# Kernel optimization log

Hardware: AMD Instinct MI355X
Metric: run time of the kernel (lower is better)

The kernel has to match this reference:

```python
import jax, jax.numpy as jnp
import numpy as np

RADIUS, HEAD, SLOT, DIM = 16.0, 8, 112, 512

def _l2norm(x, axis):
    n = jnp.linalg.norm(x, axis=axis, keepdims=True)
    return x / jnp.maximum(n, 1e-12)

def _layernorm(x, g, b, eps=1e-5):
    mu = jnp.mean(x, axis=-1, keepdims=True)
    var = jnp.mean((x - mu) ** 2, axis=-1, keepdims=True)
    return (x - mu) / jnp.sqrt(var + eps) * g + b

def setup_inputs() -> dict:
    key = jax.random.key(0)
    ks = jax.random.split(key, 12)
    B, S = 32, 512
    return {
        "query": jax.random.normal(ks[0], (B, S, DIM), jnp.float32),
        "value": jax.random.normal(ks[1], (B, S, DIM), jnp.float32),
        "key_mem": jax.random.normal(ks[2], (HEAD * SLOT, DIM // HEAD), jnp.float32) * 0.5,
        "value_mem": jax.random.normal(ks[3], (SLOT, DIM), jnp.float32) * 0.5,
        "Wq": jax.random.normal(ks[4], (DIM, DIM), jnp.float32) * 0.02,
        "bq": jnp.zeros((DIM,), jnp.float32),
        "Wv": jax.random.normal(ks[5], (DIM, DIM), jnp.float32) * 0.02,
        "bv": jnp.zeros((DIM,), jnp.float32),
        "Wl": jax.random.normal(ks[6], (DIM, DIM * HEAD), jnp.float32) * 0.02,
        "bl": jnp.zeros((DIM,), jnp.float32),
        "g1": jnp.ones((DIM,), jnp.float32), "b1": jnp.zeros((DIM,), jnp.float32),
        "g2": jnp.ones((DIM,), jnp.float32), "b2": jnp.zeros((DIM,), jnp.float32),
        "g3": jnp.ones((DIM,), jnp.float32), "b3": jnp.zeros((DIM,), jnp.float32),
    }

def reference(query, value, key_mem, value_mem, Wq, bq, Wv, bv, Wl, bl,
              g1, b1, g2, b2, g3, b3):
    B, S, C = query.shape
    mq = query.reshape(B * S, C)                                   # (BS, 512)
    # --- key addressing (read path) ---
    key_norm = _l2norm(key_mem.reshape(HEAD, SLOT, -1), axis=2)    # (h, s, 64)
    eq = _l2norm((mq @ Wq.T + bq).reshape(B * S, HEAD, -1), axis=2)
    key_sim = jnp.einsum('bhd,hsd->bhs', eq, key_norm)             # (BS, h, s)
    key_add = jax.nn.softmax(RADIUS * key_sim, axis=2)
    m_head = jnp.einsum('bhs,sd->bhd', key_add,
                        jax.lax.stop_gradient(value_mem))          # (BS, h, 512)
    vir = _layernorm(m_head.reshape(B * S, HEAD * DIM) @ Wl.T + bl, g2, b2)
    te_fusion = _layernorm(query + vir.reshape(B, S, DIM), g1, b1)  # dropout = eval identity
    # --- value addressing (write/train path) ---
    mv = value.reshape(B * S, DIM)
    ev = jax.lax.stop_gradient(mv) @ Wv.T + bv
    value_norm = _l2norm(value_mem, axis=1)                        # (s, 512)
    value_sim = _l2norm(ev, axis=1) @ value_norm.T                 # (BS, s)
    value_add = jax.nn.softmax(RADIUS * value_sim, axis=1)
    aud = value_add @ value_mem                                    # (BS, 512)
    contrastive = 0.5 * jnp.abs(jnp.eye(SLOT, dtype=value_norm.dtype)
                                - value_norm @ value_norm.T).sum()[None]
    mvd = jax.lax.stop_gradient(mv)
    cos = (aud * mvd).sum(1) / jnp.maximum(
        jnp.linalg.norm(aud, axis=1) * jnp.linalg.norm(mvd, axis=1), 1e-8)
    recon = jnp.abs(1.0 - cos).reshape(B, S).sum(1)                # (B,)
    aud = _layernorm(aud, g3, b3)
    tr_fusion = _layernorm(query + aud.reshape(B, S, DIM), g1, b1)
    return (te_fusion, tr_fusion, recon, contrastive)
```

## Files before the change

### kernel.cpp

```cpp
#include <hip/hip_runtime.h>
#include <math.h>

#define DIMC   512
#define HEADS  8
#define SLOTS  112
#define HD     64
#define NROWS  16384
#define RADIUSF 16.0f

typedef short short8 __attribute__((ext_vector_type(8)));
typedef unsigned short ushort8 __attribute__((ext_vector_type(8)));
typedef float f32x4  __attribute__((ext_vector_type(4)));

__device__ __forceinline__ unsigned short f2bf(float f)
{
    unsigned u = __float_as_uint(f);
    unsigned r = (u + 0x7FFFu + ((u >> 16) & 1u)) >> 16;
    return (unsigned short)r;
}
__device__ __forceinline__ float bf2f(unsigned short h)
{
    return __uint_as_float((unsigned)h << 16);
}

__device__ __forceinline__ void gl16(const void* g, void* lds_wave_base)
{
    __builtin_amdgcn_global_load_lds(
        (const __attribute__((address_space(1))) unsigned int*)g,
        (__attribute__((address_space(3))) unsigned int*)lds_wave_base,
        16, 0, 0);
}

#define DPP_ADD(x, ctrl, rmask)                                               \
    (x) += __int_as_float(__builtin_amdgcn_update_dpp(                        \
               0, __float_as_int(x), (ctrl), (rmask), 0xf, true))

__device__ __forceinline__ float wsum64(float x)
{
    DPP_ADD(x, 0x111, 0xf);
    DPP_ADD(x, 0x112, 0xf);
    DPP_ADD(x, 0x114, 0xf);
    DPP_ADD(x, 0x118, 0xf);
    DPP_ADD(x, 0x142, 0xa);
    DPP_ADD(x, 0x143, 0xc);
    return __int_as_float(__builtin_amdgcn_readlane(__float_as_int(x), 63));
}

__device__ __forceinline__ void wsum64_4(float& a, float& b, float& c, float& d)
{
    DPP_ADD(a, 0x111, 0xf); DPP_ADD(b, 0x111, 0xf); DPP_ADD(c, 0x111, 0xf); DPP_ADD(d, 0x111, 0xf);
    DPP_ADD(a, 0x112, 0xf); DPP_ADD(b, 0x112, 0xf); DPP_ADD(c, 0x112, 0xf); DPP_ADD(d, 0x112, 0xf);
    DPP_ADD(a, 0x114, 0xf); DPP_ADD(b, 0x114, 0xf); DPP_ADD(c, 0x114, 0xf); DPP_ADD(d, 0x114, 0xf);
    DPP_ADD(a, 0x118, 0xf); DPP_ADD(b, 0x118, 0xf); DPP_ADD(c, 0x118, 0xf); DPP_ADD(d, 0x118, 0xf);
    DPP_ADD(a, 0x142, 0xa); DPP_ADD(b, 0x142, 0xa); DPP_ADD(c, 0x142, 0xa); DPP_ADD(d, 0x142, 0xa);
    DPP_ADD(a, 0x143, 0xc); DPP_ADD(b, 0x143, 0xc); DPP_ADD(c, 0x143, 0xc); DPP_ADD(d, 0x143, 0xc);
    a = __int_as_float(__builtin_amdgcn_readlane(__float_as_int(a), 63));
    b = __int_as_float(__builtin_amdgcn_readlane(__float_as_int(b), 63));
    c = __int_as_float(__builtin_amdgcn_readlane(__float_as_int(c), 63));
    d = __int_as_float(__builtin_amdgcn_readlane(__float_as_int(d), 63));
}

__global__ __launch_bounds__(256)
void gemm_bf16(const short* __restrict__ A, int lda,
               const short* __restrict__ B, int ldb,
               float* __restrict__ C, unsigned short* __restrict__ Cb,
               int ldc, int K, const float* __restrict__ bias, int Nvalid,
               int aZ, int bZ, int cZ)
{
    __shared__ short As[128 * 32];
    __shared__ short Bs[128 * 32];
    A += (size_t)blockIdx.z * aZ;
    B += (size_t)blockIdx.z * bZ;
    const size_t czoff = (size_t)blockIdx.z * cZ;
    const int tid  = threadIdx.x;
    const int wave = tid >> 6;
    const int lane = tid & 63;
    const int m0 = blockIdx.y * 128;
    const int n0 = blockIdx.x * 128;
    const int wm = (wave >> 1) * 64;
    const int wn = (wave & 1) * 64;

    const int srow = tid >> 2;
    const int schk = (tid & 3) * 8;

    const int fr = lane & 15;
    const int fq = (lane >> 4) * 8;

    f32x4 acc[4][4] = {};

    const short* Ag = A + (size_t)(m0 + srow) * lda + schk;
    const short* Bg = B + (size_t)(n0 + srow) * ldb + schk;

    short* asL = As + wave * 512;
    short* asU = As + 2048 + wave * 512;
    short* bsL = Bs + wave * 512;
    short* bsU = Bs + 2048 + wave * 512;

    for (int k0 = 0; k0 < K; k0 += 32) {
        gl16(Ag, asL);
        gl16(Ag + (size_t)64 * lda, asU);
        gl16(Bg, bsL);
        gl16(Bg + (size_t)64 * ldb, bsU);
        Ag += 32; Bg += 32;
        __syncthreads();
        short8 af[4], bf[4];
        #pragma unroll
        for (int i = 0; i < 4; ++i)
            af[i] = *(const short8*)&As[(wm + i * 16 + fr) * 32 + fq];
        #pragma unroll
        for (int j = 0; j < 4; ++j)
            bf[j] = *(const short8*)&Bs[(wn + j * 16 + fr) * 32 + fq];
        #pragma unroll
        for (int i = 0; i < 4; ++i)
            #pragma unroll
            for (int j = 0; j < 4; ++j)
                acc[i][j] = __builtin_amdgcn_mfma_f32_16x16x32_bf16(
                    af[i], bf[j], acc[i][j], 0, 0, 0);
        __syncthreads();
    }

    const int cr = (lane >> 4) * 4;
    const int cc = lane & 15;
    #pragma unroll
    for (int i = 0; i < 4; ++i) {
        const int grow = m0 + wm + i * 16 + cr;
        #pragma unroll
        for (int j = 0; j < 4; ++j) {
            const int gcol = n0 + wn + j * 16 + cc;
            if (gcol < Nvalid) {
                const float bb = bias ? bias[gcol] : 0.f;
                const size_t base = czoff + (size_t)grow * ldc + gcol;
                #pragma unroll
                for (int r = 0; r < 4; ++r) {
                    const float val = acc[i][j][r] + bb;
                    if (C)  C[base + (size_t)r * ldc]  = val;
                    if (Cb) Cb[base + (size_t)r * ldc] = f2bf(val);
                }
            }
        }
    }
}

__global__ __launch_bounds__(256)
void gemm_softmax(const short* __restrict__ A, int lda, int aZ,
                  const short* __restrict__ B, int ldb, int bZ,
                  int K,
                  unsigned short* __restrict__ Ob, int ldo, int oPerZ, int padN)
{
    __shared__ short As[128 * 32];
    __shared__ short Bs[128 * 32];
    __shared__ float P[128][113];
    __shared__ float hinvS[128];
    A += (size_t)blockIdx.z * aZ;
    B += (size_t)blockIdx.z * bZ;
    const int tid  = threadIdx.x;
    const int wave = tid >> 6;
    const int lane = tid & 63;
    const int m0 = blockIdx.y * 128;
    const int wm = (wave >> 1) * 64;
    const int wn = (wave & 1) * 64;
    const int srow = tid >> 2;
    const int schk = (tid & 3) * 8;
    const int fr = lane & 15;
    const int fq = (lane >> 4) * 8;

    f32x4 acc[4][4] = {};
    float ss[4] = {0.f, 0.f, 0.f, 0.f};

    const short* Ag = A + (size_t)(m0 + srow) * lda + schk;
    const short* Bg = B + (size_t)srow * ldb + schk;

    short* asL = As + wave * 512;
    short* asU = As + 2048 + wave * 512;
    short* bsL = Bs + wave * 512;
    short* bsU = Bs + 2048 + wave * 512;

    for (int k0 = 0; k0 < K; k0 += 32) {
        gl16(Ag, asL);
        gl16(Ag + (size_t)64 * lda, asU);
        gl16(Bg, bsL);
        gl16(Bg + (size_t)64 * ldb, bsU);
        Ag += 32; Bg += 32;
        __syncthreads();
        short8 af[4], bf[4];
        #pragma unroll
        for (int i = 0; i < 4; ++i)
            af[i] = *(const short8*)&As[(wm + i * 16 + fr) * 32 + fq];
        #pragma unroll
        for (int j = 0; j < 4; ++j)
            bf[j] = *(const short8*)&Bs[(wn + j * 16 + fr) * 32 + fq];
        #pragma unroll
        for (int i = 0; i < 4; ++i)
            #pragma unroll
            for (int e = 0; e < 8; ++e) {
                const float f = bf2f((unsigned short)af[i][e]);
                ss[i] += f * f;
            }
        #pragma unroll
        for (int i = 0; i < 4; ++i)
            #pragma unroll
            for (int j = 0; j < 4; ++j)
                acc[i][j] = __builtin_amdgcn_mfma_f32_16x16x32_bf16(
                    af[i], bf[j], acc[i][j], 0, 0, 0);
        __syncthreads();
    }

    #pragma unroll
    for (int i = 0; i < 4; ++i) {
        ss[i] += __shfl_xor(ss[i], 16, 64);
        ss[i] += __shfl_xor(ss[i], 32, 64);
    }
    if (lane < 16) {
        #pragma unroll
        for (int i = 0; i < 4; ++i)
            hinvS[wm + i * 16 + lane] = 1.f / fmaxf(sqrtf(ss[i]), 1e-12f);
    }

    const int cr = (lane >> 4) * 4;
    const int cc = lane & 15;
    #pragma unroll
    for (int i = 0; i < 4; ++i) {
        const int prow = wm + i * 16 + cr;
        #pragma unroll
        for (int j = 0; j < 4; ++j) {
            const int pcol = wn + j * 16 + cc;
            if (pcol < SLOTS) {
                #pragma unroll
                for (int r = 0; r < 4; ++r)
                    P[prow + r][pcol] = acc[i][j][r];
            }
        }
    }
    __syncthreads();

    const int rowt = tid >> 1;
    const int half = tid & 1;
    const int k0 = half * 56;
    const int rr = m0 + rowt;
    const float s = RADIUSF * hinvS[rowt];
    float mx = -1e30f;
    for (int k = k0; k < k0 + 56; ++k) mx = fmaxf(mx, P[rowt][k]);
    mx = fmaxf(mx, __shfl_xor(mx, 1, 64));
    float sum = 0.f;
    for (int k = k0; k < k0 + 56; ++k) {
        const float e = __expf(s * (P[rowt][k] - mx));
        P[rowt][k] = e;
        sum += e;
    }
    sum += __shfl_xor(sum, 1, 64);
    const float inv = 1.f / sum;
    unsigned short* orow = Ob + (size_t)rr * ldo + (size_t)blockIdx.z * oPerZ;
    for (int k = k0; k < k0 + 56; ++k) orow[k] = f2bf(P[rowt][k] * inv);
    if (half == 1)
        for (int k = SLOTS; k < padN; ++k) orow[k] = 0;
}

__device__ __forceinline__ float block_sum_256(float v, float* red)
{
    #pragma unroll
    for (int off = 32; off; off >>= 1) v += __shfl_down(v, off, 64);
    const int lane = threadIdx.x & 63, wid = threadIdx.x >> 6;
    __syncthreads();
    if (lane == 0) red[wid] = v;
    __syncthreads();
    return red[0] + red[1] + red[2] + red[3];
}

__global__ void conv_all(const float* __restrict__ q, const float* __restrict__ v,
                         const float* __restrict__ Wq, const float* __restrict__ Wv,
                         const float* __restrict__ Wl, const float* __restrict__ vm,
                         unsigned short* __restrict__ qbf, unsigned short* __restrict__ vbf,
                         unsigned short* __restrict__ wqbf, unsigned short* __restrict__ wvbf,
                         unsigned short* __restrict__ wlbf, unsigned short* __restrict__ vmbf)
{
    const int i = blockIdx.x * blockDim.x + threadIdx.x;
    const float* src;
    unsigned short* dst;
    int off;
    if (i < 2097152)      { src = q;  dst = qbf;  off = i; }
    else if (i < 4194304) { src = v;  dst = vbf;  off = i - 2097152; }
    else if (i < 4259840) { src = Wq; dst = wqbf; off = i - 4194304; }
    else if (i < 4325376) { src = Wv; dst = wvbf; off = i - 4259840; }
    else if (i < 4849664) { src = Wl; dst = wlbf; off = i - 4325376; }
    else if (i < 4864000) { src = vm; dst = vmbf; off = i - 4849664; }
    else {
        const int j = i - 4864000;
        *(ushort4*)(vmbf + 57344 + (size_t)j * 4) = make_ushort4(0, 0, 0, 0);
        return;
    }
    const float4 x = *(const float4*)(src + (size_t)off * 4);
    ushort4 o;
    o.x = f2bf(x.x); o.y = f2bf(x.y); o.z = f2bf(x.z); o.w = f2bf(x.w);
    *(ushort4*)(dst + (size_t)off * 4) = o;
}

__global__ void prep_key_norm(const float* __restrict__ km,
                              unsigned short* __restrict__ knb,
                              float* __restrict__ outrc)
{
    const int row = blockIdx.x;
    const int h = row >> 7, s = row & 127;
    const int lane = threadIdx.x;
    if (row == 0 && lane < 33) outrc[lane] = 0.f;
    const float v = (s < SLOTS) ? km[(size_t)(h * SLOTS + s) * HD + lane] : 0.f;
    const float ssum = wsum64(v * v);
    const float inv = 1.f / fmaxf(sqrtf(ssum), 1e-12f);
    knb[(size_t)row * HD + lane] = f2bf(v * inv);
}

__global__ void prep_value_norm(const float* __restrict__ vm,
                                float* __restrict__ vn,
                                unsigned short* __restrict__ vnb,
                                unsigned short* __restrict__ vmTb)
{
    const int row = blockIdx.x;
    const int tid = threadIdx.x;
    if (row >= 112) {
        const int idx = (row - 112) * 256 + tid;
        if (idx < 8192) {
            vmTb[(size_t)(idx >> 4) * 128 + 112 + (idx & 15)] = 0;
        } else {
            const int j = idx - 8192;
            vnb[(size_t)(112 + (j >> 9)) * 512 + (j & 511)] = 0;
        }
        return;
    }
    __shared__ float red[4];
    const float v0 = vm[(size_t)row * DIMC + tid];
    const float v1 = vm[(size_t)row * DIMC + 256 + tid];
    const float tot = block_sum_256(v0 * v0 + v1 * v1, red);
    const float inv = 1.f / fmaxf(sqrtf(tot), 1e-12f);
    vn[(size_t)row * DIMC + tid]        = v0 * inv;
    vn[(size_t)row * DIMC + 256 + tid]  = v1 * inv;
    vnb[(size_t)row * DIMC + tid]       = f2bf(v0 * inv);
    vnb[(size_t)row * DIMC + 256 + tid] = f2bf(v1 * inv);
    vmTb[(size_t)tid * 128 + row]         = f2bf(v0);
    vmTb[(size_t)(256 + tid) * 128 + row] = f2bf(v1);
}

__global__ void contrastive_kernel(const float* __restrict__ vn, float* __restrict__ outc)
{
    __shared__ float vni[DIMC];
    __shared__ float red[2];
    const int i = blockIdx.x, tid = threadIdx.x;
    for (int d = tid; d < DIMC; d += 128) vni[d] = vn[(size_t)i * DIMC + d];
    __syncthreads();
    float t = 0.f;
    if (tid < SLOTS) {
        const float* r = vn + (size_t)tid * DIMC;
        float dot = 0.f;
        for (int d = 0; d < DIMC; ++d) dot += vni[d] * r[d];
        const float delta = (tid == i) ? 1.f : 0.f;
        t = fabsf(delta - dot);
    }
    #pragma unroll
    for (int off = 32; off; off >>= 1) t += __shfl_down(t, off, 64);
    if ((tid & 63) == 0) red[tid >> 6] = t;
    __syncthreads();
    if (tid == 0) atomicAdd(outc, 0.5f * (red[0] + red[1]));
}

__global__ __launch_bounds__(256, 4)
void vir_te_w(const float* __restrict__ vir_pre, const float* __restrict__ query,
              const float* __restrict__ g1, const float* __restrict__ b1,
              const float* __restrict__ g2, const float* __restrict__ b2,
              float* __restrict__ out_te)
{
    const int wave = threadIdx.x >> 6, lane = threadIdx.x & 63;
    const int r0 = blockIdx.x * 8 + wave * 2;
    const int c0 = lane * 8;

    float x[2][8], q[2][8];
    #pragma unroll
    for (int p = 0; p < 2; ++p) {
        const size_t base = (size_t)(r0 + p) * DIMC + c0;
        *(f32x4*)&x[p][0] = *(const f32x4*)(vir_pre + base);
        *(f32x4*)&x[p][4] = *(const f32x4*)(vir_pre + base + 4);
        *(f32x4*)&q[p][0] = *(const f32x4*)(query + base);
        *(f32x4*)&q[p][4] = *(const f32x4*)(query + base + 4);
    }
    float gg2[8], bb2[8], gg1[8], bb1[8];
    *(f32x4*)&gg2[0] = *(const f32x4*)(g2 + c0);
    *(f32x4*)&gg2[4] = *(const f32x4*)(g2 + c0 + 4);
    *(f32x4*)&bb2[0] = *(const f32x4*)(b2 + c0);
    *(f32x4*)&bb2[4] = *(const f32x4*)(b2 + c0 + 4);
    *(f32x4*)&gg1[0] = *(const f32x4*)(g1 + c0);
    *(f32x4*)&gg1[4] = *(const f32x4*)(g1 + c0 + 4);
    *(f32x4*)&bb1[0] = *(const f32x4*)(b1 + c0);
    *(f32x4*)&bb1[4] = *(const f32x4*)(b1 + c0 + 4);

    float s1[2] = {0.f, 0.f}, s2[2] = {0.f, 0.f};
    #pragma unroll
    for (int p = 0; p < 2; ++p)
        #pragma unroll
        for (int i = 0; i < 8; ++i) {
            s1[p] += x[p][i];
            s2[p] += x[p][i] * x[p][i];
        }
    wsum64_4(s1[0], s2[0], s1[1], s2[1]);

    float y[2][8];
    float t1[2] = {0.f, 0.f}, t2[2] = {0.f, 0.f};
    #pragma unroll
    for (int p = 0; p < 2; ++p) {
        const float mu = s1[p] * (1.f / DIMC);
        const float var = s2[p] * (1.f / DIMC) - mu * mu;
        const float rstd = rsqrtf(var + 1e-5f);
        #pragma unroll
        for (int i = 0; i < 8; ++i) {
            const float v = (x[p][i] - mu) * rstd * gg2[i] + bb2[i];
            y[p][i] = q[p][i] + v;
            t1[p] += y[p][i];
            t2[p] += y[p][i] * y[p][i];
        }
    }
    wsum64_4(t1[0], t2[0], t1[1], t2[1]);

    #pragma unroll
    for (int p = 0; p < 2; ++p) {
        const float mu = t1[p] * (1.f / DIMC);
        const float var = t2[p] * (1.f / DIMC) - mu * mu;
        const float rstd = rsqrtf(var + 1e-5f);
        float o[8];
        #pragma unroll
        for (int i = 0; i < 8; ++i)
            o[i] = (y[p][i] - mu) * rstd * gg1[i] + bb1[i];
        const size_t base = (size_t)(r0 + p) * DIMC + c0;
        *(float4*)(out_te + base)     = make_float4(o[0], o[1], o[2], o[3]);
        *(float4*)(out_te + base + 4) = make_float4(o[4], o[5], o[6], o[7]);
    }
}

__global__ __launch_bounds__(256, 4)
void aud_epilogue_w(const float* __restrict__ aud, const float* __restrict__ value,
                    const float* __restrict__ query,
                    const float* __restrict__ g1, const float* __restrict__ b1,
                    const float* __restrict__ g3, const float* __restrict__ b3,
                    float* __restrict__ out_tr, float* __restrict__ recon)
{
    __shared__ float red[4];
    const int wave = threadIdx.x >> 6, lane = threadIdx.x & 63;
    const int r0 = blockIdx.x * 8 + wave * 2;
    const int c0 = lane * 8;

    float a[2][8], v[2][8], q[2][8];
    #pragma unroll
    for (int p = 0; p < 2; ++p) {
        const size_t base = (size_t)(r0 + p) * DIMC + c0;
        *(f32x4*)&a[p][0] = *(const f32x4*)(aud + base);
        *(f32x4*)&a[p][4] = *(const f32x4*)(aud + base + 4);
        *(f32x4*)&v[p][0] = *(const f32x4*)(value + base);
        *(f32x4*)&v[p][4] = *(const f32x4*)(value + base + 4);
        *(f32x4*)&q[p][0] = *(const f32x4*)(query + base);
        *(f32x4*)&q[p][4] = *(const f32x4*)(query + base + 4);
    }
    float gg3[8], bb3[8], gg1[8], bb1[8];
    *(f32x4*)&gg3[0] = *(const f32x4*)(g3 + c0);
    *(f32x4*)&gg3[4] = *(const f32x4*)(g3 + c0 + 4);
    *(f32x4*)&bb3[0] = *(const f32x4*)(b3 + c0);
    *(f32x4*)&bb3[4] = *(const f32x4*)(b3 + c0 + 4);
    *(f32x4*)&gg1[0] = *(const f32x4*)(g1 + c0);
    *(f32x4*)&gg1[4] = *(const f32x4*)(g1 + c0 + 4);
    *(f32x4*)&bb1[0] = *(const f32x4*)(b1 + c0);
    *(f32x4*)&bb1[4] = *(const f32x4*)(b1 + c0 + 4);

    float dot[2] = {0.f, 0.f}, na[2] = {0.f, 0.f};
    float nv[2] = {0.f, 0.f}, s1[2] = {0.f, 0.f};
    #pragma unroll
    for (int p = 0; p < 2; ++p)
        #pragma unroll
        for (int i = 0; i < 8; ++i) {
            dot[p] += a[p][i] * v[p][i];
            na[p]  += a[p][i] * a[p][i];
            nv[p]  += v[p][i] * v[p][i];
            s1[p]  += a[p][i];
        }
    wsum64_4(dot[0], na[0], nv[0], s1[0]);
    wsum64_4(dot[1], na[1], nv[1], s1[1]);

    float rloc = 0.f;
    #pragma unroll
    for (int p = 0; p < 2; ++p) {
        const float cosv = dot[p] / fmaxf(sqrtf(na[p]) * sqrtf(nv[p]), 1e-8f);
        rloc += fabsf(1.f - cosv);
    }
    if (lane == 0) red[wave] = rloc;

    float y[2][8];
    float t1[2] = {0.f, 0.f}, t2[2] = {0.f, 0.f};
    #pragma unroll
    for (int p = 0; p < 2; ++p) {
        const float mu = s1[p] * (1.f / DIMC);
        const float var = na[p] * (1.f / DIMC) - mu * mu;
        const float rstd = rsqrtf(var + 1e-5f);
        #pragma unroll
        for (int i = 0; i < 8; ++i) {
            const float w = (a[p][i] - mu) * rstd * gg3[i] + bb3[i];
            y[p][i] = q[p][i] + w;
            t1[p] += y[p][i];
            t2[p] += y[p][i] * y[p][i];
        }
    }
    wsum64_4(t1[0], t2[0], t1[1], t2[1]);

    #pragma unroll
    for (int p = 0; p < 2; ++p) {
        const float mu = t1[p] * (1.f / DIMC);
        const float var = t2[p] * (1.f / DIMC) - mu * mu;
        const float rstd = rsqrtf(var + 1e-5f);
        float o[8];
        #pragma unroll
        for (int i = 0; i < 8; ++i)
            o[i] = (y[p][i] - mu) * rstd * gg1[i] + bb1[i];
        const size_t base = (size_t)(r0 + p) * DIMC + c0;
        *(float4*)(out_tr + base)     = make_float4(o[0], o[1], o[2], o[3]);
        *(float4*)(out_tr + base + 4) = make_float4(o[4], o[5], o[6], o[7]);
    }

    __syncthreads();
    if (threadIdx.x == 0)
        atomicAdd(&recon[r0 >> 9], red[0] + red[1] + red[2] + red[3]);
}

extern "C" void kernel_launch(void* const* d_in, const int* in_sizes, int n_in,
                              void* d_out, int out_size, void* d_ws, size_t ws_size,
                              hipStream_t stream)
{
    const float* query = (const float*)d_in[0];
    const float* value = (const float*)d_in[1];
    const float* keym  = (const float*)d_in[2];
    const float* vmem  = (const float*)d_in[3];
    const float* Wq    = (const float*)d_in[4];
    const float* bq    = (const float*)d_in[5];
    const float* Wv    = (const float*)d_in[6];
    const float* bv    = (const float*)d_in[7];
    const float* Wl    = (const float*)d_in[8];
    const float* bl    = (const float*)d_in[9];
    const float* g1    = (const float*)d_in[10];
    const float* b1    = (const float*)d_in[11];
    const float* g2    = (const float*)d_in[12];
    const float* b2    = (const float*)d_in[13];
    const float* g3    = (const float*)d_in[14];
    const float* b3    = (const float*)d_in[15];

    float* out    = (float*)d_out;
    float* out_te = out;
    float* out_tr = out + 8388608;
    float* out_rc = out + 16777216;

    float* ws = (float*)d_ws;
    unsigned short* w_knb  = (unsigned short*)(ws + 0);
    unsigned short* w_vmTb = (unsigned short*)(ws + 32768);
    unsigned short* w_vnb  = (unsigned short*)(ws + 65536);
    float*          w_vn   = ws + 98304;
    unsigned short* w_w2tbf= (unsigned short*)(ws + 155648);
    unsigned short* w_vmbf = (unsigned short*)(ws + 516096);
    unsigned short* w_wlbf = (unsigned short*)(ws + 548864);
    float*          w_big1 = ws + 1597440;
    unsigned short* w_xbf  = (unsigned short*)(ws + 9986048);
    unsigned short* w_kaddc= (unsigned short*)(ws + 14180352);
    unsigned short* w_vsb  = (unsigned short*)(ws + 21520384);
    unsigned short* w_qbf  = (unsigned short*)(ws + 22568960);
    unsigned short* w_vbf  = (unsigned short*)(ws + 26763264);
    unsigned short* w_wqbf = (unsigned short*)(ws + 30957568);
    unsigned short* w_wvbf = (unsigned short*)(ws + 31088640);

    conv_all<<<19008, 256, 0, stream>>>(query, value, Wq, Wv, Wl, vmem,
                                        w_qbf, w_vbf, w_wqbf, w_wvbf,
                                        w_wlbf, w_vmbf);
    prep_key_norm<<<1024, 64, 0, stream>>>(keym, w_knb, out_rc);
    prep_value_norm<<<176, 256, 0, stream>>>(vmem, w_vn, w_vnb, w_vmTb);
    contrastive_kernel<<<112, 128, 0, stream>>>(w_vn, out_rc + 32);
    gemm_bf16<<<dim3(1, 4, 8), 256, 0, stream>>>(
        (const short*)w_wlbf, HEADS * DIMC, (const short*)w_vmbf, DIMC,
        nullptr, w_w2tbf, HEADS * SLOTS, DIMC, nullptr, SLOTS,
        DIMC, 0, SLOTS);

    gemm_bf16<<<dim3(4, 128), 256, 0, stream>>>(
        (const short*)w_qbf, DIMC, (const short*)w_wqbf, DIMC,
        nullptr, w_xbf, DIMC, DIMC, bq, DIMC, 0, 0, 0);
    gemm_softmax<<<dim3(1, 128, 8), 256, 0, stream>>>(
        (const short*)w_xbf, DIMC, HD, (const short*)w_knb, HD, 128 * HD,
        HD, w_kaddc, HEADS * SLOTS, SLOTS, SLOTS);
    gemm_bf16<<<dim3(4, 128), 256, 0, stream>>>(
        (const short*)w_kaddc, HEADS * SLOTS, (const short*)w_w2tbf, HEADS * SLOTS,
        w_big1, nullptr, DIMC, HEADS * SLOTS, bl, DIMC, 0, 0, 0);
    vir_te_w<<<NROWS / 8, 256, 0, stream>>>(w_big1, query, g1, b1, g2, b2, out_te);

    gemm_bf16<<<dim3(4, 128), 256, 0, stream>>>(
        (const short*)w_vbf, DIMC, (const short*)w_wvbf, DIMC,
        nullptr, w_xbf, DIMC, DIMC, bv, DIMC, 0, 0, 0);
    gemm_softmax<<<dim3(1, 128, 1), 256, 0, stream>>>(
        (const short*)w_xbf, DIMC, 0, (const short*)w_vnb, DIMC, 0,
        DIMC, w_vsb, 128, 0, 128);
    gemm_bf16<<<dim3(4, 128), 256, 0, stream>>>(
        (const short*)w_vsb, 128, (const short*)w_vmTb, 128,
        w_big1, nullptr, DIMC, 128, nullptr, DIMC, 0, 0, 0);
    aud_epilogue_w<<<NROWS / 8, 256, 0, stream>>>(
        w_big1, value, query, g1, b1, g3, b3, out_tr, out_rc);
}
```

Measured before the change: 359.8 us.

## Fuse output GEMMs with layernorm epilogues into full-row-tile kernels

```diff
diff --git a/kernel.cpp b/kernel.cpp
--- a/kernel.cpp
+++ b/kernel.cpp
@@ -255,6 +255,246 @@
         for (int k = SLOTS; k < padN; ++k) orow[k] = 0;
 }
 
+
+#define FUSED_GEMM_CORE(A, lda, B, ldb, K)                                    \
+    f32x4 acc[2][8] = {};                                                     \
+    {                                                                         \
+        const int lrow = lane >> 2;                                           \
+        const int lchk = (lane & 3) * 8;                                      \
+        const short* Ag = (A) + (size_t)(m0 + wave * 16 + lrow) * (lda) + lchk;\
+        const short* Bg = (B) + (size_t)(wave * 16 + lrow) * (ldb) + lchk;    \
+        short* asB = As + wave * 512;                                         \
+        short* bsB = Bs + wave * 512;                                         \
+        for (int k0 = 0; k0 < (K); k0 += 32) {                                \
+            if (wave < 2) gl16(Ag, asB);                                      \
+            _Pragma("unroll")                                                 \
+            for (int s = 0; s < 8; ++s)                                       \
+                gl16(Bg + (size_t)(s * 64) * (ldb), bsB + s * 2048);          \
+            Ag += 32; Bg += 32;                                               \
+            __syncthreads();                                                  \
+            short8 af[2], bf[8];                                              \
+            af[0] = *(const short8*)&As[fr * 32 + fq];                        \
+            af[1] = *(const short8*)&As[(16 + fr) * 32 + fq];                 \
+            _Pragma("unroll")                                                 \
+            for (int c = 0; c < 8; ++c)                                       \
+                bf[c] = *(const short8*)&Bs[(wave * 128 + c * 16 + fr) * 32 + fq];\
+            _Pragma("unroll")                                                 \
+            for (int i = 0; i < 2; ++i)                                       \
+                _Pragma("unroll")                                             \
+                for (int c = 0; c < 8; ++c)                                   \
+                    acc[i][c] = __builtin_amdgcn_mfma_f32_16x16x32_bf16(      \
+                        af[i], bf[c], acc[i][c], 0, 0, 0);                    \
+            __syncthreads();                                                  \
+        }                                                                     \
+    }                                                                         \
+    {                                                                         \
+        const int cr = (lane >> 4) * 4;                                       \
+        const int cc = lane & 15;                                             \
+        _Pragma("unroll")                                                     \
+        for (int i = 0; i < 2; ++i)                                           \
+            _Pragma("unroll")                                                 \
+            for (int c = 0; c < 8; ++c) {                                     \
+                const int col = wave * 128 + c * 16 + cc;                     \
+                _Pragma("unroll")                                             \
+                for (int r = 0; r < 4; ++r)                                   \
+                    P[(i * 16 + cr + r) * 516 + col] = acc[i][c][r];          \
+            }                                                                 \
+    }                                                                         \
+    __syncthreads();
+
+__global__ __launch_bounds__(256)
+void gemm_vir_te(const short* __restrict__ A, int lda,
+                 const short* __restrict__ B, int ldb, int K,
+                 const float* __restrict__ bias, const float* __restrict__ query,
+                 const float* __restrict__ g1, const float* __restrict__ b1,
+                 const float* __restrict__ g2, const float* __restrict__ b2,
+                 float* __restrict__ out_te)
+{
+    __shared__ float P[32 * 516];
+    short* As = (short*)P;
+    short* Bs = As + 1024;
+    const int tid = threadIdx.x;
+    const int wave = tid >> 6;
+    const int lane = tid & 63;
+    const int m0 = blockIdx.x * 32;
+    const int fr = lane & 15;
+    const int fq = (lane >> 4) * 8;
+
+    FUSED_GEMM_CORE(A, lda, B, ldb, K)
+
+    const int c0 = lane * 8;
+    float blv[8], gg2[8], bb2[8], gg1[8], bb1[8];
+    *(f32x4*)&blv[0] = *(const f32x4*)(bias + c0);
+    *(f32x4*)&blv[4] = *(const f32x4*)(bias + c0 + 4);
+    *(f32x4*)&gg2[0] = *(const f32x4*)(g2 + c0);
+    *(f32x4*)&gg2[4] = *(const f32x4*)(g2 + c0 + 4);
+    *(f32x4*)&bb2[0] = *(const f32x4*)(b2 + c0);
+    *(f32x4*)&bb2[4] = *(const f32x4*)(b2 + c0 + 4);
+    *(f32x4*)&gg1[0] = *(const f32x4*)(g1 + c0);
+    *(f32x4*)&gg1[4] = *(const f32x4*)(g1 + c0 + 4);
+    *(f32x4*)&bb1[0] = *(const f32x4*)(b1 + c0);
+    *(f32x4*)&bb1[4] = *(const f32x4*)(b1 + c0 + 4);
+
+    for (int rp = 0; rp < 4; ++rp) {
+        const int lr0 = rp * 8 + wave * 2;
+        float x[2][8], q[2][8];
+        #pragma unroll
+        for (int p = 0; p < 2; ++p) {
+            *(f32x4*)&x[p][0] = *(const f32x4*)&P[(lr0 + p) * 516 + c0];
+            *(f32x4*)&x[p][4] = *(const f32x4*)&P[(lr0 + p) * 516 + c0 + 4];
+            const size_t gbase = (size_t)(m0 + lr0 + p) * DIMC + c0;
+            *(f32x4*)&q[p][0] = *(const f32x4*)(query + gbase);
+            *(f32x4*)&q[p][4] = *(const f32x4*)(query + gbase + 4);
+            #pragma unroll
+            for (int j = 0; j < 8; ++j) x[p][j] += blv[j];
+        }
+        float s1[2] = {0.f, 0.f}, s2[2] = {0.f, 0.f};
+        #pragma unroll
+        for (int p = 0; p < 2; ++p)
+            #pragma unroll
+            for (int j = 0; j < 8; ++j) {
+                s1[p] += x[p][j];
+                s2[p] += x[p][j] * x[p][j];
+            }
+        wsum64_4(s1[0], s2[0], s1[1], s2[1]);
+
+        float y[2][8];
+        float t1[2] = {0.f, 0.f}, t2[2] = {0.f, 0.f};
+        #pragma unroll
+        for (int p = 0; p < 2; ++p) {
+            const float mu = s1[p] * (1.f / DIMC);
+            const float var = s2[p] * (1.f / DIMC) - mu * mu;
+            const float rstd = rsqrtf(var + 1e-5f);
+            #pragma unroll
+            for (int j = 0; j < 8; ++j) {
+                const float v = (x[p][j] - mu) * rstd * gg2[j] + bb2[j];
+                y[p][j] = q[p][j] + v;
+                t1[p] += y[p][j];
+                t2[p] += y[p][j] * y[p][j];
+            }
+        }
+        wsum64_4(t1[0], t2[0], t1[1], t2[1]);
+
+        #pragma unroll
+        for (int p = 0; p < 2; ++p) {
+            const float mu = t1[p] * (1.f / DIMC);
+            const float var = t2[p] * (1.f / DIMC) - mu * mu;
+            const float rstd = rsqrtf(var + 1e-5f);
+            float o[8];
+            #pragma unroll
+            for (int j = 0; j < 8; ++j)
+                o[j] = (y[p][j] - mu) * rstd * gg1[j] + bb1[j];
+            const size_t gbase = (size_t)(m0 + lr0 + p) * DIMC + c0;
+            *(float4*)(out_te + gbase)     = make_float4(o[0], o[1], o[2], o[3]);
+            *(float4*)(out_te + gbase + 4) = make_float4(o[4], o[5], o[6], o[7]);
+        }
+    }
+}
+
+__global__ __launch_bounds__(256)
+void gemm_aud_tr(const short* __restrict__ A, int lda,
+                 const short* __restrict__ B, int ldb, int K,
+                 const float* __restrict__ value, const float* __restrict__ query,
+                 const float* __restrict__ g1, const float* __restrict__ b1,
+                 const float* __restrict__ g3, const float* __restrict__ b3,
+                 float* __restrict__ out_tr, float* __restrict__ recon)
+{
+    __shared__ float P[32 * 516];
+    __shared__ float red[4];
+    short* As = (short*)P;
+    short* Bs = As + 1024;
+    const int tid = threadIdx.x;
+    const int wave = tid >> 6;
+    const int lane = tid & 63;
+    const int m0 = blockIdx.x * 32;
+    const int fr = lane & 15;
+    const int fq = (lane >> 4) * 8;
+
+    FUSED_GEMM_CORE(A, lda, B, ldb, K)
+
+    const int c0 = lane * 8;
+    float gg3[8], bb3[8], gg1[8], bb1[8];
+    *(f32x4*)&gg3[0] = *(const f32x4*)(g3 + c0);
+    *(f32x4*)&gg3[4] = *(const f32x4*)(g3 + c0 + 4);
+    *(f32x4*)&bb3[0] = *(const f32x4*)(b3 + c0);
+    *(f32x4*)&bb3[4] = *(const f32x4*)(b3 + c0 + 4);
+    *(f32x4*)&gg1[0] = *(const f32x4*)(g1 + c0);
+    *(f32x4*)&gg1[4] = *(const f32x4*)(g1 + c0 + 4);
+    *(f32x4*)&bb1[0] = *(const f32x4*)(b1 + c0);
+    *(f32x4*)&bb1[4] = *(const f32x4*)(b1 + c0 + 4);
+
+    float rloc = 0.f;
+    for (int rp = 0; rp < 4; ++rp) {
+        const int lr0 = rp * 8 + wave * 2;
+        float a[2][8], v[2][8], q[2][8];
+        #pragma unroll
+        for (int p = 0; p < 2; ++p) {
+            *(f32x4*)&a[p][0] = *(const f32x4*)&P[(lr0 + p) * 516 + c0];
+            *(f32x4*)&a[p][4] = *(const f32x4*)&P[(lr0 + p) * 516 + c0 + 4];
+            const size_t gbase = (size_t)(m0 + lr0 + p) * DIMC + c0;
+            *(f32x4*)&v[p][0] = *(const f32x4*)(value + gbase);
+            *(f32x4*)&v[p][4] = *(const f32x4*)(value + gbase + 4);
+            *(f32x4*)&q[p][0] = *(const f32x4*)(query + gbase);
+            *(f32x4*)&q[p][4] = *(const f32x4*)(query + gbase + 4);
+        }
+        float dot[2] = {0.f, 0.f}, na[2] = {0.f, 0.f};
+        float nv[2] = {0.f, 0.f}, s1[2] = {0.f, 0.f};
+        #pragma unroll
+        for (int p = 0; p < 2; ++p)
+            #pragma unroll
+            for (int j = 0; j < 8; ++j) {
+                dot[p] += a[p][j] * v[p][j];
+                na[p]  += a[p][j] * a[p][j];
+                nv[p]  += v[p][j] * v[p][j];
+                s1[p]  += a[p][j];
+            }
+        wsum64_4(dot[0], na[0], nv[0], s1[0]);
+        wsum64_4(dot[1], na[1], nv[1], s1[1]);
+
+        #pragma unroll
+        for (int p = 0; p < 2; ++p) {
+            const float cosv = dot[p] / fmaxf(sqrtf(na[p]) * sqrtf(nv[p]), 1e-8f);
+            rloc += fabsf(1.f - cosv);
+        }
+
+        float y[2][8];
+        float t1[2] = {0.f, 0.f}, t2[2] = {0.f, 0.f};
+        #pragma unroll
+        for (int p = 0; p < 2; ++p) {
+            const float mu = s1[p] * (1.f / DIMC);
+            const float var = na[p] * (1.f / DIMC) - mu * mu;
+            const float rstd = rsqrtf(var + 1e-5f);
+            #pragma unroll
+            for (int j = 0; j < 8; ++j) {
+                const float w = (a[p][j] - mu) * rstd * gg3[j] + bb3[j];
+                y[p][j] = q[p][j] + w;
+                t1[p] += y[p][j];
+                t2[p] += y[p][j] * y[p][j];
+            }
+        }
+        wsum64_4(t1[0], t2[0], t1[1], t2[1]);
+
+        #pragma unroll
+        for (int p = 0; p < 2; ++p) {
+            const float mu = t1[p] * (1.f / DIMC);
+            const float var = t2[p] * (1.f / DIMC) - mu * mu;
+            const float rstd = rsqrtf(var + 1e-5f);
+            float o[8];
+            #pragma unroll
+            for (int j = 0; j < 8; ++j)
+                o[j] = (y[p][j] - mu) * rstd * gg1[j] + bb1[j];
+            const size_t gbase = (size_t)(m0 + lr0 + p) * DIMC + c0;
+            *(float4*)(out_tr + gbase)     = make_float4(o[0], o[1], o[2], o[3]);
+            *(float4*)(out_tr + gbase + 4) = make_float4(o[4], o[5], o[6], o[7]);
+        }
+    }
+
+    if (lane == 0) red[wave] = rloc;
+    __syncthreads();
+    if (tid == 0)
+        atomicAdd(&recon[m0 >> 9], red[0] + red[1] + red[2] + red[3]);
+}
+
 __device__ __forceinline__ float block_sum_256(float v, float* red)
 {
     #pragma unroll
@@ -358,168 +598,6 @@
     if ((tid & 63) == 0) red[tid >> 6] = t;
     __syncthreads();
     if (tid == 0) atomicAdd(outc, 0.5f * (red[0] + red[1]));
-}
-
-__global__ __launch_bounds__(256, 4)
-void vir_te_w(const float* __restrict__ vir_pre, const float* __restrict__ query,
-              const float* __restrict__ g1, const float* __restrict__ b1,
-              const float* __restrict__ g2, const float* __restrict__ b2,
-              float* __restrict__ out_te)
-{
-    const int wave = threadIdx.x >> 6, lane = threadIdx.x & 63;
-    const int r0 = blockIdx.x * 8 + wave * 2;
-    const int c0 = lane * 8;
-
-    float x[2][8], q[2][8];
-    #pragma unroll
-    for (int p = 0; p < 2; ++p) {
-        const size_t base = (size_t)(r0 + p) * DIMC + c0;
-        *(f32x4*)&x[p][0] = *(const f32x4*)(vir_pre + base);
-        *(f32x4*)&x[p][4] = *(const f32x4*)(vir_pre + base + 4);
-        *(f32x4*)&q[p][0] = *(const f32x4*)(query + base);
-        *(f32x4*)&q[p][4] = *(const f32x4*)(query + base + 4);
-    }
-    float gg2[8], bb2[8], gg1[8], bb1[8];
-    *(f32x4*)&gg2[0] = *(const f32x4*)(g2 + c0);
-    *(f32x4*)&gg2[4] = *(const f32x4*)(g2 + c0 + 4);
-    *(f32x4*)&bb2[0] = *(const f32x4*)(b2 + c0);
-    *(f32x4*)&bb2[4] = *(const f32x4*)(b2 + c0 + 4);
-    *(f32x4*)&gg1[0] = *(const f32x4*)(g1 + c0);
-    *(f32x4*)&gg1[4] = *(const f32x4*)(g1 + c0 + 4);
-    *(f32x4*)&bb1[0] = *(const f32x4*)(b1 + c0);
-    *(f32x4*)&bb1[4] = *(const f32x4*)(b1 + c0 + 4);
-
-    float s1[2] = {0.f, 0.f}, s2[2] = {0.f, 0.f};
-    #pragma unroll
-    for (int p = 0; p < 2; ++p)
-        #pragma unroll
-        for (int i = 0; i < 8; ++i) {
-            s1[p] += x[p][i];
-            s2[p] += x[p][i] * x[p][i];
-        }
-    wsum64_4(s1[0], s2[0], s1[1], s2[1]);
-
-    float y[2][8];
-    float t1[2] = {0.f, 0.f}, t2[2] = {0.f, 0.f};
-    #pragma unroll
-    for (int p = 0; p < 2; ++p) {
-        const float mu = s1[p] * (1.f / DIMC);
-        const float var = s2[p] * (1.f / DIMC) - mu * mu;
-        const float rstd = rsqrtf(var + 1e-5f);
-        #pragma unroll
-        for (int i = 0; i < 8; ++i) {
-            const float v = (x[p][i] - mu) * rstd * gg2[i] + bb2[i];
-            y[p][i] = q[p][i] + v;
-            t1[p] += y[p][i];
-            t2[p] += y[p][i] * y[p][i];
-        }
-    }
-    wsum64_4(t1[0], t2[0], t1[1], t2[1]);
-
-    #pragma unroll
-    for (int p = 0; p < 2; ++p) {
-        const float mu = t1[p] * (1.f / DIMC);
-        const float var = t2[p] * (1.f / DIMC) - mu * mu;
-        const float rstd = rsqrtf(var + 1e-5f);
-        float o[8];
-        #pragma unroll
-        for (int i = 0; i < 8; ++i)
-            o[i] = (y[p][i] - mu) * rstd * gg1[i] + bb1[i];
-        const size_t base = (size_t)(r0 + p) * DIMC + c0;
-        *(float4*)(out_te + base)     = make_float4(o[0], o[1], o[2], o[3]);
-        *(float4*)(out_te + base + 4) = make_float4(o[4], o[5], o[6], o[7]);
-    }
-}
-
-__global__ __launch_bounds__(256, 4)
-void aud_epilogue_w(const float* __restrict__ aud, const float* __restrict__ value,
-                    const float* __restrict__ query,
-                    const float* __restrict__ g1, const float* __restrict__ b1,
-                    const float* __restrict__ g3, const float* __restrict__ b3,
-                    float* __restrict__ out_tr, float* __restrict__ recon)
-{
-    __shared__ float red[4];
-    const int wave = threadIdx.x >> 6, lane = threadIdx.x & 63;
-    const int r0 = blockIdx.x * 8 + wave * 2;
-    const int c0 = lane * 8;
-
-    float a[2][8], v[2][8], q[2][8];
-    #pragma unroll
-    for (int p = 0; p < 2; ++p) {
-        const size_t base = (size_t)(r0 + p) * DIMC + c0;
-        *(f32x4*)&a[p][0] = *(const f32x4*)(aud + base);
-        *(f32x4*)&a[p][4] = *(const f32x4*)(aud + base + 4);
-        *(f32x4*)&v[p][0] = *(const f32x4*)(value + base);
-        *(f32x4*)&v[p][4] = *(const f32x4*)(value + base + 4);
-        *(f32x4*)&q[p][0] = *(const f32x4*)(query + base);
-        *(f32x4*)&q[p][4] = *(const f32x4*)(query + base + 4);
-    }
-    float gg3[8], bb3[8], gg1[8], bb1[8];
-    *(f32x4*)&gg3[0] = *(const f32x4*)(g3 + c0);
-    *(f32x4*)&gg3[4] = *(const f32x4*)(g3 + c0 + 4);
-    *(f32x4*)&bb3[0] = *(const f32x4*)(b3 + c0);
-    *(f32x4*)&bb3[4] = *(const f32x4*)(b3 + c0 + 4);
-    *(f32x4*)&gg1[0] = *(const f32x4*)(g1 + c0);
-    *(f32x4*)&gg1[4] = *(const f32x4*)(g1 + c0 + 4);
-    *(f32x4*)&bb1[0] = *(const f32x4*)(b1 + c0);
-    *(f32x4*)&bb1[4] = *(const f32x4*)(b1 + c0 + 4);
-
-    float dot[2] = {0.f, 0.f}, na[2] = {0.f, 0.f};
-    float nv[2] = {0.f, 0.f}, s1[2] = {0.f, 0.f};
-    #pragma unroll
-    for (int p = 0; p < 2; ++p)
-        #pragma unroll
-        for (int i = 0; i < 8; ++i) {
-            dot[p] += a[p][i] * v[p][i];
-            na[p]  += a[p][i] * a[p][i];
-            nv[p]  += v[p][i] * v[p][i];
-            s1[p]  += a[p][i];
-        }
-    wsum64_4(dot[0], na[0], nv[0], s1[0]);
-    wsum64_4(dot[1], na[1], nv[1], s1[1]);
-
-    float rloc = 0.f;
-    #pragma unroll
-    for (int p = 0; p < 2; ++p) {
-        const float cosv = dot[p] / fmaxf(sqrtf(na[p]) * sqrtf(nv[p]), 1e-8f);
-        rloc += fabsf(1.f - cosv);
-    }
-    if (lane == 0) red[wave] = rloc;
-
-    float y[2][8];
-    float t1[2] = {0.f, 0.f}, t2[2] = {0.f, 0.f};
-    #pragma unroll
-    for (int p = 0; p < 2; ++p) {
-        const float mu = s1[p] * (1.f / DIMC);
-        const float var = na[p] * (1.f / DIMC) - mu * mu;
-        const float rstd = rsqrtf(var + 1e-5f);
-        #pragma unroll
-        for (int i = 0; i < 8; ++i) {
-            const float w = (a[p][i] - mu) * rstd * gg3[i] + bb3[i];
-            y[p][i] = q[p][i] + w;
-            t1[p] += y[p][i];
-            t2[p] += y[p][i] * y[p][i];
-        }
-    }
-    wsum64_4(t1[0], t2[0], t1[1], t2[1]);
-
-    #pragma unroll
-    for (int p = 0; p < 2; ++p) {
-        const float mu = t1[p] * (1.f / DIMC);
-        const float var = t2[p] * (1.f / DIMC) - mu * mu;
-        const float rstd = rsqrtf(var + 1e-5f);
-        float o[8];
-        #pragma unroll
-        for (int i = 0; i < 8; ++i)
-            o[i] = (y[p][i] - mu) * rstd * gg1[i] + bb1[i];
-        const size_t base = (size_t)(r0 + p) * DIMC + c0;
-        *(float4*)(out_tr + base)     = make_float4(o[0], o[1], o[2], o[3]);
-        *(float4*)(out_tr + base + 4) = make_float4(o[4], o[5], o[6], o[7]);
-    }
-
-    __syncthreads();
-    if (threadIdx.x == 0)
-        atomicAdd(&recon[r0 >> 9], red[0] + red[1] + red[2] + red[3]);
 }
 
 extern "C" void kernel_launch(void* const* d_in, const int* in_sizes, int n_in,
@@ -554,16 +632,15 @@
     unsigned short* w_vnb  = (unsigned short*)(ws + 65536);
     float*          w_vn   = ws + 98304;
     unsigned short* w_w2tbf= (unsigned short*)(ws + 155648);
-    unsigned short* w_vmbf = (unsigned short*)(ws + 516096);
-    unsigned short* w_wlbf = (unsigned short*)(ws + 548864);
-    float*          w_big1 = ws + 1597440;
-    unsigned short* w_xbf  = (unsigned short*)(ws + 9986048);
-    unsigned short* w_kaddc= (unsigned short*)(ws + 14180352);
-    unsigned short* w_vsb  = (unsigned short*)(ws + 21520384);
-    unsigned short* w_qbf  = (unsigned short*)(ws + 22568960);
-    unsigned short* w_vbf  = (unsigned short*)(ws + 26763264);
-    unsigned short* w_wqbf = (unsigned short*)(ws + 30957568);
-    unsigned short* w_wvbf = (unsigned short*)(ws + 31088640);
+    unsigned short* w_vmbf = (unsigned short*)(ws + 385024);
+    unsigned short* w_wlbf = (unsigned short*)(ws + 417792);
+    unsigned short* w_xbf  = (unsigned short*)(ws + 1466368);
+    unsigned short* w_kaddc= (unsigned short*)(ws + 5660672);
+    unsigned short* w_vsb  = (unsigned short*)(ws + 13000704);
+    unsigned short* w_qbf  = (unsigned short*)(ws + 14049280);
+    unsigned short* w_vbf  = (unsigned short*)(ws + 18243584);
+    unsigned short* w_wqbf = (unsigned short*)(ws + 22437888);
+    unsigned short* w_wvbf = (unsigned short*)(ws + 22568960);
 
     conv_all<<<19008, 256, 0, stream>>>(query, value, Wq, Wv, Wl, vmem,
                                         w_qbf, w_vbf, w_wqbf, w_wvbf,
@@ -582,10 +659,9 @@
     gemm_softmax<<<dim3(1, 128, 8), 256, 0, stream>>>(
         (const short*)w_xbf, DIMC, HD, (const short*)w_knb, HD, 128 * HD,
         HD, w_kaddc, HEADS * SLOTS, SLOTS, SLOTS);
-    gemm_bf16<<<dim3(4, 128), 256, 0, stream>>>(
+    gemm_vir_te<<<NROWS / 32, 256, 0, stream>>>(
         (const short*)w_kaddc, HEADS * SLOTS, (const short*)w_w2tbf, HEADS * SLOTS,
-        w_big1, nullptr, DIMC, HEADS * SLOTS, bl, DIMC, 0, 0, 0);
-    vir_te_w<<<NROWS / 8, 256, 0, stream>>>(w_big1, query, g1, b1, g2, b2, out_te);
+        HEADS * SLOTS, bl, query, g1, b1, g2, b2, out_te);
 
     gemm_bf16<<<dim3(4, 128), 256, 0, stream>>>(
         (const short*)w_vbf, DIMC, (const short*)w_wvbf, DIMC,
@@ -593,9 +669,7 @@
     gemm_softmax<<<dim3(1, 128, 1), 256, 0, stream>>>(
         (const short*)w_xbf, DIMC, 0, (const short*)w_vnb, DIMC, 0,
         DIMC, w_vsb, 128, 0, 128);
-    gemm_bf16<<<dim3(4, 128), 256, 0, stream>>>(
-        (const short*)w_vsb, 128, (const short*)w_vmTb, 128,
-        w_big1, nullptr, DIMC, 128, nullptr, DIMC, 0, 0, 0);
-    aud_epilogue_w<<<NROWS / 8, 256, 0, stream>>>(
-        w_big1, value, query, g1, b1, g3, b3, out_tr, out_rc);
-}
+    gemm_aud_tr<<<NROWS / 32, 256, 0, stream>>>(
+        (const short*)w_vsb, 128, (const short*)w_vmTb, 128, 128,
+        value, query, g1, b1, g3, b3, out_tr, out_rc);
+}
```

New measurement: 336.8 us. 1.07x faster.
